# Performance work log

Measured on AMD Instinct MI355X. Metric: run time of the kernel, lower is better.

## Reference

```python
import jax, jax.numpy as jnp
import numpy as np

C = 256      # channels
H = 8        # num_heads
D = C // H   # head_dim = 32
B = 8        # packed segments (events)
LQ = 256     # queries per event
LKV = 1024   # kv tokens per event
EPS = float(np.finfo(np.float32).eps)  # torch RMSNorm default eps (None -> dtype eps)


def rmsnorm(x, w):
    # matches torch nn.RMSNorm (applied in fp32 in Block)
    return x * jax.lax.rsqrt(jnp.mean(x * x, axis=-1, keepdims=True) + EPS) * w


def setup_inputs() -> dict:
    key = jax.random.key(0)
    ks = jax.random.split(key, 20)
    Nq, Nkv = B * LQ, B * LKV
    def w(k, shape, scale=0.05):
        return jax.random.normal(k, shape, jnp.float32) * scale
    return {
        "q": jax.random.normal(ks[0], (Nq, C), jnp.float32),
        "kv": jax.random.normal(ks[1], (Nkv, C), jnp.float32),
        "pos_q": jax.random.normal(ks[2], (Nq, C), jnp.float32),
        "pos_k": jax.random.normal(ks[3], (Nkv, C), jnp.float32),
        # RMSNorm weights
        "w_norm_kv": jnp.ones((C,), jnp.float32),
        "w_norm1": jnp.ones((C,), jnp.float32),
        "w_norm2": jnp.ones((C,), jnp.float32),
        "w_norm3": jnp.ones((C,), jnp.float32),
        # cross-attention (q_proj/k_proj/v_proj no bias; out proj has bias)  W:[out,in]
        "ca_wq": w(ks[4], (C, C)), "ca_wk": w(ks[5], (C, C)), "ca_wv": w(ks[6], (C, C)),
        "ca_wo": w(ks[7], (C, C)), "ca_bo": jnp.zeros((C,), jnp.float32),
        # self-attention (q: [C,C]; kv fused: [2C,C]; out proj has bias)
        "sa_wq": w(ks[8], (C, C)), "sa_wkv": w(ks[9], (2 * C, C)),
        "sa_wo": w(ks[10], (C, C)), "sa_bo": jnp.zeros((C,), jnp.float32),
        # MLP (hidden = 4*C)
        "mlp_w1": w(ks[11], (4 * C, C)), "mlp_b1": jnp.zeros((4 * C,), jnp.float32),
        "mlp_w2": w(ks[12], (C, 4 * C)), "mlp_b2": jnp.zeros((C,), jnp.float32),
        # packed varlen metadata
        "cu_seqlens_q": jnp.arange(B + 1, dtype=jnp.int32) * LQ,
        "cu_seqlens_kv": jnp.arange(B + 1, dtype=jnp.int32) * LKV,
        "max_seqlen_q": LQ,
        "max_seqlen_kv": LKV,
    }


def reference(q, kv, pos_q, pos_k,
              w_norm_kv, w_norm1, w_norm2, w_norm3,
              ca_wq, ca_wk, ca_wv, ca_wo, ca_bo,
              sa_wq, sa_wkv, sa_wo, sa_bo,
              mlp_w1, mlp_b1, mlp_w2, mlp_b2,
              cu_seqlens_q, cu_seqlens_kv, max_seqlen_q, max_seqlen_kv):
    scale = D ** -0.5
    kv_n = rmsnorm(kv, w_norm_kv)

    # ---- cross-attention (use_attn_mask=False -> no mask, full packed attention) ----
    q_n = rmsnorm(q, w_norm1)
    qc = ((q_n + pos_q) @ ca_wq.T).reshape(-1, H, D)   # [Nq,H,D]
    kc = ((kv_n + pos_k) @ ca_wk.T).reshape(-1, H, D)  # [Nkv,H,D]
    vc = (kv_n @ ca_wv.T).reshape(-1, H, D)
    s = jnp.einsum('nhd,mhd->hnm', qc, kc) * scale     # [H,Nq,Nkv]
    feat = jnp.einsum('hnm,mhd->nhd', jax.nn.softmax(s, axis=-1), vc).reshape(-1, C)
    x = q + (feat @ ca_wo.T + ca_bo)

    # ---- self-attention with block-diagonal mask from cu_seqlens_q ----
    x_n = rmsnorm(x, w_norm2)
    qs = ((x_n + pos_q) @ sa_wq.T).reshape(-1, H, D)
    kvs = (x_n @ sa_wkv.T).reshape(-1, 2, H, D)
    ks_, vs = kvs[:, 0], kvs[:, 1]
    n = x.shape[0]
    seg = jnp.searchsorted(cu_seqlens_q[1:], jnp.arange(n, dtype=cu_seqlens_q.dtype), side='right')
    bias = jnp.where(seg[:, None] == seg[None, :], 0.0, -10000.0)  # [Nq,Nq]
    s2 = jnp.einsum('nhd,mhd->hnm', qs, ks_) * scale + bias
    feat2 = jnp.einsum('hnm,mhd->nhd', jax.nn.softmax(s2, axis=-1), vs).reshape(-1, C)
    x = x + (feat2 @ sa_wo.T + sa_bo)

    # ---- MLP (exact GELU, as torch nn.GELU default) ----
    x_n3 = rmsnorm(x, w_norm3)
    h = jax.nn.gelu(x_n3 @ mlp_w1.T + mlp_b1, approximate=False)
    x = x + (h @ mlp_w2.T + mlp_b2)
    return x
```

## Files before the change

### kernel.cpp

```cpp
#include <hip/hip_runtime.h>
#include <cmath>


#define EPS_F 1.1920928955078125e-07f

typedef __attribute__((ext_vector_type(8))) short short8;
typedef __attribute__((ext_vector_type(4))) short short4v;
typedef __attribute__((ext_vector_type(4))) float f32x4;

__device__ __forceinline__ unsigned short f2bf(float v) {
    union { float f; unsigned int u; } c; c.f = v;
    unsigned int r = c.u + 0x7FFFu + ((c.u >> 16) & 1u);
    return (unsigned short)(r >> 16);
}
__device__ __forceinline__ float bf2f(unsigned short u) {
    union { unsigned int u; float f; } c; c.u = ((unsigned int)u) << 16;
    return c.f;
}

struct WPtrs { const float* p[16]; };

__global__ __launch_bounds__(256) void cast_weights_kernel(
    WPtrs wp, unsigned short* __restrict__ outw)
{
    const int unit = blockIdx.x >> 5;
    const int off = ((blockIdx.x & 31) * 256 + threadIdx.x) * 8;
    const float* src = wp.p[unit];
    const float4 v0 = *(const float4*)(src + off);
    const float4 v1 = *(const float4*)(src + off + 4);
    short8 o;
    o[0] = (short)f2bf(v0.x); o[1] = (short)f2bf(v0.y);
    o[2] = (short)f2bf(v0.z); o[3] = (short)f2bf(v0.w);
    o[4] = (short)f2bf(v1.x); o[5] = (short)f2bf(v1.y);
    o[6] = (short)f2bf(v1.z); o[7] = (short)f2bf(v1.w);
    *(short8*)(outw + unit * 65536 + off) = o;
}

__global__ __launch_bounds__(256) void rmsnorm_dual_kernel(
    const float* __restrict__ X, const float* __restrict__ W,
    const float* __restrict__ pos, unsigned short* __restrict__ out_plain,
    unsigned short* __restrict__ out_pos)
{
    const int row = blockIdx.x;
    const int tid = threadIdx.x;
    const size_t base = (size_t)row * 256;
    const float v = X[base + tid];
    float sq = v * v;
    #pragma unroll
    for (int m = 1; m < 64; m <<= 1) sq += __shfl_xor(sq, m);
    __shared__ float ws4[4];
    if ((tid & 63) == 0) ws4[tid >> 6] = sq;
    __syncthreads();
    const float total = ws4[0] + ws4[1] + ws4[2] + ws4[3];
    const float ms = total * (1.0f / 256.0f) + EPS_F;
    float inv = rsqrtf(ms);
    inv = inv * (1.5f - 0.5f * ms * inv * inv);
    const float xn = v * inv * W[tid];
    if (out_plain) out_plain[base + tid] = f2bf(xn);
    if (out_pos)   out_pos[base + tid] = f2bf(xn + pos[base + tid]);
}

template<int ACT, int HAS_BIAS, int HAS_RES, int OUT_BF16>
__global__ __launch_bounds__(256) void gemm_bf16_kernel(
    const unsigned short* __restrict__ A, const unsigned short* __restrict__ Bw,
    const float* __restrict__ bias, const float* __restrict__ res,
    void* __restrict__ Cout, int M, int N, int K, float oscale)
{
    __shared__ __align__(16) char As[64 * 128];
    __shared__ __align__(16) char Bs[64 * 128];
    const int bm = blockIdx.x * 64, bn = blockIdx.y * 64;
    const int tid = threadIdx.x;
    const int w = tid >> 6, l = tid & 63;
    const int ql = l & 15, b = l >> 4;
    const int wr = w >> 1, wc = w & 1;

    f32x4 acc[2][2];
    #pragma unroll
    for (int m = 0; m < 2; ++m)
        #pragma unroll
        for (int n = 0; n < 2; ++n) acc[m][n] = (f32x4){0.f, 0.f, 0.f, 0.f};

    const int srow = tid >> 3;
    const int scolb = (tid & 7) * 16;
    const unsigned short* Ap0 = A + (size_t)(bm + srow) * K + (tid & 7) * 8;
    const unsigned short* Ap1 = A + (size_t)(bm + srow + 32) * K + (tid & 7) * 8;
    const unsigned short* Bp0 = Bw + (size_t)(bn + srow) * K + (tid & 7) * 8;
    const unsigned short* Bp1 = Bw + (size_t)(bn + srow + 32) * K + (tid & 7) * 8;
    const int sw0 = (srow * 128 + scolb) ^ ((srow & 7) << 4);
    const int sw1 = ((srow + 32) * 128 + scolb) ^ ((srow & 7) << 4);

    short8 ra0 = *(const short8*)(Ap0);
    short8 ra1 = *(const short8*)(Ap1);
    short8 rb0 = *(const short8*)(Bp0);
    short8 rb1 = *(const short8*)(Bp1);

    for (int k0 = 0; k0 < K; k0 += 64) {
        __syncthreads();
        *(short8*)(As + sw0) = ra0;
        *(short8*)(As + sw1) = ra1;
        *(short8*)(Bs + sw0) = rb0;
        *(short8*)(Bs + sw1) = rb1;
        if (k0 + 64 < K) {
            ra0 = *(const short8*)(Ap0 + k0 + 64);
            ra1 = *(const short8*)(Ap1 + k0 + 64);
            rb0 = *(const short8*)(Bp0 + k0 + 64);
            rb1 = *(const short8*)(Bp1 + k0 + 64);
        }
        __syncthreads();
        #pragma unroll
        for (int ks = 0; ks < 2; ++ks) {
            short8 af[2], bfr[2];
            #pragma unroll
            for (int m = 0; m < 2; ++m) {
                const int row = wr * 32 + m * 16 + ql;
                af[m] = *(const short8*)(As + ((row * 128 + ks * 64 + b * 16) ^ ((row & 7) << 4)));
            }
            #pragma unroll
            for (int n = 0; n < 2; ++n) {
                const int row = wc * 32 + n * 16 + ql;
                bfr[n] = *(const short8*)(Bs + ((row * 128 + ks * 64 + b * 16) ^ ((row & 7) << 4)));
            }
            #pragma unroll
            for (int m = 0; m < 2; ++m)
                #pragma unroll
                for (int n = 0; n < 2; ++n)
                    acc[m][n] = __builtin_amdgcn_mfma_f32_16x16x32_bf16(af[m], bfr[n], acc[m][n], 0, 0, 0);
        }
    }

    #pragma unroll
    for (int m = 0; m < 2; ++m) {
        #pragma unroll
        for (int n = 0; n < 2; ++n) {
            const int col = bn + wc * 32 + n * 16 + ql;
            #pragma unroll
            for (int r = 0; r < 4; ++r) {
                const int row = bm + wr * 32 + m * 16 + 4 * b + r;
                float v = acc[m][n][r];
                if (HAS_BIAS) v += bias[col];
                if (HAS_RES)  v += res[(size_t)row * N + col];
                if (ACT == 1) v = 0.5f * v * (1.0f + erff(v * 0.7071067811865476f));
                if (OUT_BF16)
                    ((unsigned short*)Cout)[(size_t)row * N + col] = f2bf(v * oscale);
                else
                    ((float*)Cout)[(size_t)row * N + col] = v;
            }
        }
    }
}

template<int SELF>
__global__ __launch_bounds__(256) void flash_mfma_kernel(
    const unsigned short* __restrict__ Qb, const unsigned short* __restrict__ Kb,
    const unsigned short* __restrict__ Vb, float* __restrict__ part_o,
    float* __restrict__ part_ml, unsigned short* __restrict__ out_bf,
    int kv_stride, int kv_per_split)
{
    __shared__ __align__(16) unsigned short Ks[64 * 32];
    __shared__ __align__(16) unsigned short Vt[32 * 64];
    const int qtile = blockIdx.x, h = blockIdx.y, split = blockIdx.z;
    const int tid = threadIdx.x;
    const int w = tid >> 6, l = tid & 63;
    const int ql = l & 15, b = l >> 4;
    const int qrow = qtile * 64 + w * 16 + ql;

    short8 qfrag = *(const short8*)(Qb + (size_t)qrow * 256 + h * 32 + b * 8);

    f32x4 oacc0 = {0.f, 0.f, 0.f, 0.f};
    f32x4 oacc1 = {0.f, 0.f, 0.f, 0.f};
    float m_run = -3.0e38f, l_part = 0.f;

    const int kv_base = SELF ? ((qtile >> 2) << 8) : split * kv_per_split;
    const int ntiles = kv_per_split / 64;
    const int skv = tid >> 2;
    const int sd8 = (tid & 3) * 8;

    for (int t = 0; t < ntiles; ++t) {
        const int kvg = kv_base + t * 64;
        short8 kin = *(const short8*)(Kb + (size_t)(kvg + skv) * kv_stride + h * 32 + sd8);
        short8 vin = *(const short8*)(Vb + (size_t)(kvg + skv) * kv_stride + h * 32 + sd8);
        __syncthreads();
        *(short8*)(Ks + skv * 32 + sd8) = kin;
        #pragma unroll
        for (int j = 0; j < 8; ++j) {
            const int d = sd8 + j;
            const int hh = (d + (d >> 3)) & 7;
            Vt[d * 64 + (skv ^ (hh << 3))] = (unsigned short)vin[j];
        }
        __syncthreads();

        f32x4 s[4];
        #pragma unroll
        for (int j = 0; j < 4; ++j) {
            short8 kfrag = *(const short8*)(Ks + (j * 16 + ql) * 32 + b * 8);
            f32x4 z = {0.f, 0.f, 0.f, 0.f};
            s[j] = __builtin_amdgcn_mfma_f32_16x16x32_bf16(kfrag, qfrag, z, 0, 0, 0);
        }

        float tmax = s[0][0];
        #pragma unroll
        for (int j = 0; j < 4; ++j)
            #pragma unroll
            for (int i = 0; i < 4; ++i) tmax = fmaxf(tmax, s[j][i]);
        tmax = fmaxf(tmax, __shfl_xor(tmax, 16));
        tmax = fmaxf(tmax, __shfl_xor(tmax, 32));
        const float newm = fmaxf(m_run, tmax);
        const float r = __expf(m_run - newm);
        m_run = newm;

        float p[4][4];
        float psum = 0.f;
        #pragma unroll
        for (int j = 0; j < 4; ++j)
            #pragma unroll
            for (int i = 0; i < 4; ++i) {
                p[j][i] = __expf(s[j][i] - newm);
                psum += p[j][i];
            }
        l_part = l_part * r + psum;
        #pragma unroll
        for (int i = 0; i < 4; ++i) { oacc0[i] *= r; oacc1[i] *= r; }

        short8 pf0, pf1;
        #pragma unroll
        for (int e = 0; e < 8; ++e) {
            pf0[e] = (short)f2bf(p[(e >> 2)][e & 3]);
            pf1[e] = (short)f2bf(p[2 + (e >> 2)][e & 3]);
        }

        #pragma unroll
        for (int tt = 0; tt < 2; ++tt) {
            const int d = 16 * tt + ql;
            const int hh = (d + (d >> 3)) & 7;
            #pragma unroll
            for (int c = 0; c < 2; ++c) {
                short4v lo = *(const short4v*)(Vt + d * 64 + ((32 * c + 4 * b) ^ (hh << 3)));
                short4v hi = *(const short4v*)(Vt + d * 64 + ((32 * c + 16 + 4 * b) ^ (hh << 3)));
                short8 vfrag;
                #pragma unroll
                for (int e = 0; e < 4; ++e) { vfrag[e] = lo[e]; vfrag[e + 4] = hi[e]; }
                if (tt == 0)
                    oacc0 = __builtin_amdgcn_mfma_f32_16x16x32_bf16(vfrag, (c == 0) ? pf0 : pf1, oacc0, 0, 0, 0);
                else
                    oacc1 = __builtin_amdgcn_mfma_f32_16x16x32_bf16(vfrag, (c == 0) ? pf0 : pf1, oacc1, 0, 0, 0);
            }
        }
    }

    float lsum = l_part;
    lsum += __shfl_xor(lsum, 16);
    lsum += __shfl_xor(lsum, 32);

    if (SELF) {
        const float invl = 1.0f / lsum;
        unsigned short* op = out_bf + (size_t)qrow * 256 + h * 32;
        #pragma unroll
        for (int i = 0; i < 4; ++i) {
            op[4 * b + i]      = f2bf(oacc0[i] * invl);
            op[16 + 4 * b + i] = f2bf(oacc1[i] * invl);
        }
    } else {
        const size_t obase = ((size_t)split * 2048 + qrow) * 256 + h * 32;
        *(float4*)(part_o + obase + 4 * b)      = make_float4(oacc0[0], oacc0[1], oacc0[2], oacc0[3]);
        *(float4*)(part_o + obase + 16 + 4 * b) = make_float4(oacc1[0], oacc1[1], oacc1[2], oacc1[3]);
        if (b == 0) {
            float* mlp = part_ml + (((size_t)split * 2048 + qrow) * 8 + h) * 2;
            mlp[0] = m_run; mlp[1] = lsum;
        }
    }
}

__global__ __launch_bounds__(256) void merge_kernel(
    const float* __restrict__ part_o, const float* __restrict__ part_ml,
    unsigned short* __restrict__ feat)
{
    const int row = blockIdx.x, c = threadIdx.x;
    const int h = c >> 5;
    float m_s[4], l_s[4];
    float M = -3.0e38f;
    #pragma unroll
    for (int s = 0; s < 4; ++s) {
        const float* mlp = part_ml + (((size_t)s * 2048 + row) * 8 + h) * 2;
        m_s[s] = mlp[0]; l_s[s] = mlp[1];
        M = fmaxf(M, m_s[s]);
    }
    float num = 0.f, den = 0.f;
    #pragma unroll
    for (int s = 0; s < 4; ++s) {
        const float wgt = __expf(m_s[s] - M);
        den += wgt * l_s[s];
        num += wgt * part_o[((size_t)s * 2048 + row) * 256 + c];
    }
    feat[(size_t)row * 256 + c] = f2bf(num / den);
}

extern "C" void kernel_launch(void* const* d_in, const int* in_sizes, int n_in,
                              void* d_out, int out_size, void* d_ws, size_t ws_size,
                              hipStream_t stream)
{
    const float* q         = (const float*)d_in[0];
    const float* kv        = (const float*)d_in[1];
    const float* pos_q     = (const float*)d_in[2];
    const float* pos_k     = (const float*)d_in[3];
    const float* w_norm_kv = (const float*)d_in[4];
    const float* w_norm1   = (const float*)d_in[5];
    const float* w_norm2   = (const float*)d_in[6];
    const float* w_norm3   = (const float*)d_in[7];
    const float* ca_wq     = (const float*)d_in[8];
    const float* ca_wk     = (const float*)d_in[9];
    const float* ca_wv     = (const float*)d_in[10];
    const float* ca_wo     = (const float*)d_in[11];
    const float* ca_bo     = (const float*)d_in[12];
    const float* sa_wq     = (const float*)d_in[13];
    const float* sa_wkv    = (const float*)d_in[14];
    const float* sa_wo     = (const float*)d_in[15];
    const float* sa_bo     = (const float*)d_in[16];
    const float* mlp_w1    = (const float*)d_in[17];
    const float* mlp_b1    = (const float*)d_in[18];
    const float* mlp_w2    = (const float*)d_in[19];
    const float* mlp_b2    = (const float*)d_in[20];
    float* out = (float*)d_out;
    float* ws  = (float*)d_ws;

    unsigned short* wbf      = (unsigned short*)(ws);
    unsigned short* kvn_bf   = (unsigned short*)(ws +  524288);
    unsigned short* kvpk_bf  = (unsigned short*)(ws + 1572864);
    unsigned short* kc_bf    = (unsigned short*)(ws + 2621440);
    unsigned short* vc_bf    = (unsigned short*)(ws + 3670016);
    unsigned short* qpn_bf   = (unsigned short*)(ws + 4718592);
    unsigned short* qc_bf    = (unsigned short*)(ws + 4980736);
    float*          part_o   = ws + 5242880;
    float*          part_ml  = ws + 7340032;
    unsigned short* feat_bf  = (unsigned short*)(ws + 7471104);
    float*          x        = ws + 7733248;
    unsigned short* xn2_bf   = (unsigned short*)(ws + 8257536);
    unsigned short* xn2p_bf  = (unsigned short*)(ws + 8519680);
    unsigned short* qs_bf    = (unsigned short*)(ws + 8781824);
    unsigned short* kvs_bf   = (unsigned short*)(ws + 9043968);
    unsigned short* feat2_bf = (unsigned short*)(ws + 9568256);
    float*          x2       = ws + 9830400;
    unsigned short* xn3_bf   = (unsigned short*)(ws + 10354688);
    unsigned short* hbuf_bf  = (unsigned short*)(ws + 10616832);

    unsigned short* wq_bf     = wbf;
    unsigned short* wk_bf     = wbf + 65536;
    unsigned short* wv_bf     = wbf + 131072;
    unsigned short* wo_bf     = wbf + 196608;
    unsigned short* sa_wq_bf  = wbf + 262144;
    unsigned short* sa_wkv_bf = wbf + 327680;
    unsigned short* sa_wo_bf  = wbf + 458752;
    unsigned short* mlp_w1_bf = wbf + 524288;
    unsigned short* mlp_w2_bf = wbf + 786432;

    WPtrs wp;
    wp.p[0] = ca_wq;  wp.p[1] = ca_wk;  wp.p[2] = ca_wv;  wp.p[3] = ca_wo;
    wp.p[4] = sa_wq;  wp.p[5] = sa_wkv; wp.p[6] = sa_wkv + 65536;
    wp.p[7] = sa_wo;
    wp.p[8] = mlp_w1;           wp.p[9]  = mlp_w1 + 65536;
    wp.p[10] = mlp_w1 + 131072; wp.p[11] = mlp_w1 + 196608;
    wp.p[12] = mlp_w2;          wp.p[13] = mlp_w2 + 65536;
    wp.p[14] = mlp_w2 + 131072; wp.p[15] = mlp_w2 + 196608;

    const float qscale = 0.17677669529663687f;

    cast_weights_kernel<<<512, 256, 0, stream>>>(wp, wbf);
    rmsnorm_dual_kernel<<<8192, 256, 0, stream>>>(kv, w_norm_kv, pos_k, kvn_bf, kvpk_bf);
    rmsnorm_dual_kernel<<<2048, 256, 0, stream>>>(q, w_norm1, pos_q, nullptr, qpn_bf);
    gemm_bf16_kernel<0,0,0,1><<<dim3( 32, 4), 256, 0, stream>>>(qpn_bf,  wq_bf, nullptr, nullptr, qc_bf, 2048, 256, 256, qscale);
    gemm_bf16_kernel<0,0,0,1><<<dim3(128, 4), 256, 0, stream>>>(kvpk_bf, wk_bf, nullptr, nullptr, kc_bf, 8192, 256, 256, 1.0f);
    gemm_bf16_kernel<0,0,0,1><<<dim3(128, 4), 256, 0, stream>>>(kvn_bf,  wv_bf, nullptr, nullptr, vc_bf, 8192, 256, 256, 1.0f);
    flash_mfma_kernel<0><<<dim3(32, 8, 4), 256, 0, stream>>>(qc_bf, kc_bf, vc_bf, part_o, part_ml, nullptr, 256, 2048);
    merge_kernel<<<2048, 256, 0, stream>>>(part_o, part_ml, feat_bf);
    gemm_bf16_kernel<0,1,1,0><<<dim3(32, 4), 256, 0, stream>>>(feat_bf, wo_bf, ca_bo, q, x, 2048, 256, 256, 1.0f);
    rmsnorm_dual_kernel<<<2048, 256, 0, stream>>>(x, w_norm2, pos_q, xn2_bf, xn2p_bf);
    gemm_bf16_kernel<0,0,0,1><<<dim3(32, 4), 256, 0, stream>>>(xn2p_bf, sa_wq_bf,  nullptr, nullptr, qs_bf,  2048, 256, 256, qscale);
    gemm_bf16_kernel<0,0,0,1><<<dim3(32, 8), 256, 0, stream>>>(xn2_bf,  sa_wkv_bf, nullptr, nullptr, kvs_bf, 2048, 512, 256, 1.0f);
    flash_mfma_kernel<1><<<dim3(32, 8, 1), 256, 0, stream>>>(qs_bf, kvs_bf, kvs_bf + 256, nullptr, nullptr, feat2_bf, 512, 256);
    gemm_bf16_kernel<0,1,1,0><<<dim3(32, 4), 256, 0, stream>>>(feat2_bf, sa_wo_bf, sa_bo, x, x2, 2048, 256, 256, 1.0f);
    rmsnorm_dual_kernel<<<2048, 256, 0, stream>>>(x2, w_norm3, nullptr, xn3_bf, nullptr);
    gemm_bf16_kernel<1,1,0,1><<<dim3(32,16), 256, 0, stream>>>(xn3_bf,  mlp_w1_bf, mlp_b1, nullptr, hbuf_bf, 2048, 1024, 256, 1.0f);
    gemm_bf16_kernel<0,1,1,0><<<dim3(32, 4), 256, 0, stream>>>(hbuf_bf, mlp_w2_bf, mlp_b2, x2, out, 2048, 256, 1024, 1.0f);
}
```

Measured before the change: 234.3 us.

## Pre-swizzle K/V into MFMA fragment layout, prefetch tiles, lazy rescale softmax

The K and V projection GEMMs now write their outputs directly in a per-head, per-64-token tile layout that matches the swizzled LDS fragment layout. The flash kernel can then copy tiles with plain 16-byte loads instead of doing a scalar transposed V scatter, and it prefetches the next tile into registers. The online softmax moves to exp2 with log2e folded into the query scale, and it skips the rescale when the max grows by no more than 8. The cross-attention KV split goes from 4 to 8, which doubles the partial buffers and the merge work. The costs are more scattered GEMM epilogue stores and a larger workspace.

```diff
diff --git a/kernel.cpp b/kernel.cpp
--- a/kernel.cpp
+++ b/kernel.cpp
@@ -1,11 +1,11 @@
 #include <hip/hip_runtime.h>
+#include <hip/hip_bf16.h>
 #include <cmath>
 
 
 #define EPS_F 1.1920928955078125e-07f
 
 typedef __attribute__((ext_vector_type(8))) short short8;
-typedef __attribute__((ext_vector_type(4))) short short4v;
 typedef __attribute__((ext_vector_type(4))) float f32x4;
 
 __device__ __forceinline__ unsigned short f2bf(float v) {
@@ -13,9 +13,27 @@
     unsigned int r = c.u + 0x7FFFu + ((c.u >> 16) & 1u);
     return (unsigned short)(r >> 16);
 }
-__device__ __forceinline__ float bf2f(unsigned short u) {
-    union { unsigned int u; float f; } c; c.u = ((unsigned int)u) << 16;
-    return c.f;
+__device__ __forceinline__ unsigned short f2bf_n(float v) {
+    union { __hip_bfloat16 h; unsigned short u; } cv;
+    cv.h = __float2bfloat16(v);
+    return cv.u;
+}
+
+__device__ __forceinline__ size_t kfrag_idx(int kv, int col, int Gk) {
+    const int h = col >> 5, d = col & 31;
+    const int g = kv >> 6, row = kv & 63;
+    const int idx = (row * 32 + d) ^ ((row & 7) << 3);
+    return ((size_t)(h * Gk + g)) * 2048 + idx;
+}
+__device__ __forceinline__ size_t vfrag_idx(int kv, int col, int Gk) {
+    const int h = col >> 5, d = col & 31;
+    const int tt = d >> 4, qd = d & 15;
+    const int g = kv >> 6, r6 = kv & 63;
+    const int c = r6 >> 5, r5 = r6 & 31;
+    const int hi = r5 >> 4, lo4 = r5 & 15;
+    const int b = lo4 >> 2, e = (hi << 2) | (lo4 & 3);
+    const int idx = tt * 1024 + ((qd * 64 + c * 32 + b * 8 + e) ^ ((qd & 7) << 3));
+    return ((size_t)(h * Gk + g)) * 2048 + idx;
 }
 
 struct WPtrs { const float* p[16]; };
@@ -60,11 +78,12 @@
     if (out_pos)   out_pos[base + tid] = f2bf(xn + pos[base + tid]);
 }
 
-template<int ACT, int HAS_BIAS, int HAS_RES, int OUT_BF16>
+template<int ACT, int HAS_BIAS, int HAS_RES, int STORE>
 __global__ __launch_bounds__(256) void gemm_bf16_kernel(
     const unsigned short* __restrict__ A, const unsigned short* __restrict__ Bw,
     const float* __restrict__ bias, const float* __restrict__ res,
-    void* __restrict__ Cout, int M, int N, int K, float oscale)
+    void* __restrict__ Cout, void* __restrict__ Cout2,
+    int M, int N, int K, float oscale, int Gk)
 {
     __shared__ __align__(16) char As[64 * 128];
     __shared__ __align__(16) char Bs[64 * 128];
@@ -140,10 +159,20 @@
                 if (HAS_BIAS) v += bias[col];
                 if (HAS_RES)  v += res[(size_t)row * N + col];
                 if (ACT == 1) v = 0.5f * v * (1.0f + erff(v * 0.7071067811865476f));
-                if (OUT_BF16)
+                if (STORE == 0)
+                    ((float*)Cout)[(size_t)row * N + col] = v;
+                else if (STORE == 1)
                     ((unsigned short*)Cout)[(size_t)row * N + col] = f2bf(v * oscale);
-                else
-                    ((float*)Cout)[(size_t)row * N + col] = v;
+                else if (STORE == 2)
+                    ((unsigned short*)Cout)[kfrag_idx(row, col, Gk)] = f2bf(v * oscale);
+                else if (STORE == 3)
+                    ((unsigned short*)Cout)[vfrag_idx(row, col, Gk)] = f2bf(v * oscale);
+                else {
+                    if (col < 256)
+                        ((unsigned short*)Cout)[kfrag_idx(row, col, Gk)] = f2bf(v);
+                    else
+                        ((unsigned short*)Cout2)[vfrag_idx(row, col - 256, Gk)] = f2bf(v);
+                }
             }
         }
     }
@@ -151,13 +180,13 @@
 
 template<int SELF>
 __global__ __launch_bounds__(256) void flash_mfma_kernel(
-    const unsigned short* __restrict__ Qb, const unsigned short* __restrict__ Kb,
-    const unsigned short* __restrict__ Vb, float* __restrict__ part_o,
+    const unsigned short* __restrict__ Qb, const unsigned short* __restrict__ Kp,
+    const unsigned short* __restrict__ Vp, float* __restrict__ part_o,
     float* __restrict__ part_ml, unsigned short* __restrict__ out_bf,
-    int kv_stride, int kv_per_split)
-{
-    __shared__ __align__(16) unsigned short Ks[64 * 32];
-    __shared__ __align__(16) unsigned short Vt[32 * 64];
+    int Gk, int ntiles)
+{
+    __shared__ __align__(16) unsigned short Kt[2048];
+    __shared__ __align__(16) unsigned short Vt[2048];
     const int qtile = blockIdx.x, h = blockIdx.y, split = blockIdx.z;
     const int tid = threadIdx.x;
     const int w = tid >> 6, l = tid & 63;
@@ -166,35 +195,38 @@
 
     short8 qfrag = *(const short8*)(Qb + (size_t)qrow * 256 + h * 32 + b * 8);
 
+    const int g0 = SELF ? ((qtile >> 2) << 2) : split * ntiles;
+    const unsigned short* Ksrc = Kp + ((size_t)(h * Gk + g0)) * 2048 + tid * 8;
+    const unsigned short* Vsrc = Vp + ((size_t)(h * Gk + g0)) * 2048 + tid * 8;
+
+    const int xsw = (ql & 7) << 3;
+    const int kb  = (ql * 32 + b * 8) ^ xsw;
+    const int vb0 = (ql * 64 + b * 8) ^ xsw;
+    const int vb1 = (ql * 64 + 32 + b * 8) ^ xsw;
+
     f32x4 oacc0 = {0.f, 0.f, 0.f, 0.f};
     f32x4 oacc1 = {0.f, 0.f, 0.f, 0.f};
     float m_run = -3.0e38f, l_part = 0.f;
 
-    const int kv_base = SELF ? ((qtile >> 2) << 8) : split * kv_per_split;
-    const int ntiles = kv_per_split / 64;
-    const int skv = tid >> 2;
-    const int sd8 = (tid & 3) * 8;
+    short8 kpre = *(const short8*)Ksrc;
+    short8 vpre = *(const short8*)Vsrc;
 
     for (int t = 0; t < ntiles; ++t) {
-        const int kvg = kv_base + t * 64;
-        short8 kin = *(const short8*)(Kb + (size_t)(kvg + skv) * kv_stride + h * 32 + sd8);
-        short8 vin = *(const short8*)(Vb + (size_t)(kvg + skv) * kv_stride + h * 32 + sd8);
         __syncthreads();
-        *(short8*)(Ks + skv * 32 + sd8) = kin;
-        #pragma unroll
-        for (int j = 0; j < 8; ++j) {
-            const int d = sd8 + j;
-            const int hh = (d + (d >> 3)) & 7;
-            Vt[d * 64 + (skv ^ (hh << 3))] = (unsigned short)vin[j];
+        *(short8*)(Kt + tid * 8) = kpre;
+        *(short8*)(Vt + tid * 8) = vpre;
+        if (t + 1 < ntiles) {
+            kpre = *(const short8*)(Ksrc + (size_t)(t + 1) * 2048);
+            vpre = *(const short8*)(Vsrc + (size_t)(t + 1) * 2048);
         }
         __syncthreads();
 
         f32x4 s[4];
         #pragma unroll
         for (int j = 0; j < 4; ++j) {
-            short8 kfrag = *(const short8*)(Ks + (j * 16 + ql) * 32 + b * 8);
+            short8 kf = *(const short8*)(Kt + kb + j * 512);
             f32x4 z = {0.f, 0.f, 0.f, 0.f};
-            s[j] = __builtin_amdgcn_mfma_f32_16x16x32_bf16(kfrag, qfrag, z, 0, 0, 0);
+            s[j] = __builtin_amdgcn_mfma_f32_16x16x32_bf16(kf, qfrag, z, 0, 0, 0);
         }
 
         float tmax = s[0][0];
@@ -204,9 +236,15 @@
             for (int i = 0; i < 4; ++i) tmax = fmaxf(tmax, s[j][i]);
         tmax = fmaxf(tmax, __shfl_xor(tmax, 16));
         tmax = fmaxf(tmax, __shfl_xor(tmax, 32));
-        const float newm = fmaxf(m_run, tmax);
-        const float r = __expf(m_run - newm);
-        m_run = newm;
+
+        if (!__all(tmax <= m_run + 8.f)) {
+            const float newm = fmaxf(m_run, tmax);
+            const float r = exp2f(m_run - newm);
+            l_part *= r;
+            #pragma unroll
+            for (int i = 0; i < 4; ++i) { oacc0[i] *= r; oacc1[i] *= r; }
+            m_run = newm;
+        }
 
         float p[4][4];
         float psum = 0.f;
@@ -214,37 +252,26 @@
         for (int j = 0; j < 4; ++j)
             #pragma unroll
             for (int i = 0; i < 4; ++i) {
-                p[j][i] = __expf(s[j][i] - newm);
+                p[j][i] = exp2f(s[j][i] - m_run);
                 psum += p[j][i];
             }
-        l_part = l_part * r + psum;
-        #pragma unroll
-        for (int i = 0; i < 4; ++i) { oacc0[i] *= r; oacc1[i] *= r; }
+        l_part += psum;
 
         short8 pf0, pf1;
         #pragma unroll
         for (int e = 0; e < 8; ++e) {
-            pf0[e] = (short)f2bf(p[(e >> 2)][e & 3]);
-            pf1[e] = (short)f2bf(p[2 + (e >> 2)][e & 3]);
-        }
-
-        #pragma unroll
-        for (int tt = 0; tt < 2; ++tt) {
-            const int d = 16 * tt + ql;
-            const int hh = (d + (d >> 3)) & 7;
-            #pragma unroll
-            for (int c = 0; c < 2; ++c) {
-                short4v lo = *(const short4v*)(Vt + d * 64 + ((32 * c + 4 * b) ^ (hh << 3)));
-                short4v hi = *(const short4v*)(Vt + d * 64 + ((32 * c + 16 + 4 * b) ^ (hh << 3)));
-                short8 vfrag;
-                #pragma unroll
-                for (int e = 0; e < 4; ++e) { vfrag[e] = lo[e]; vfrag[e + 4] = hi[e]; }
-                if (tt == 0)
-                    oacc0 = __builtin_amdgcn_mfma_f32_16x16x32_bf16(vfrag, (c == 0) ? pf0 : pf1, oacc0, 0, 0, 0);
-                else
-                    oacc1 = __builtin_amdgcn_mfma_f32_16x16x32_bf16(vfrag, (c == 0) ? pf0 : pf1, oacc1, 0, 0, 0);
-            }
-        }
+            pf0[e] = (short)f2bf_n(p[(e >> 2)][e & 3]);
+            pf1[e] = (short)f2bf_n(p[2 + (e >> 2)][e & 3]);
+        }
+
+        short8 v00 = *(const short8*)(Vt + vb0);
+        short8 v01 = *(const short8*)(Vt + vb1);
+        short8 v10 = *(const short8*)(Vt + 1024 + vb0);
+        short8 v11 = *(const short8*)(Vt + 1024 + vb1);
+        oacc0 = __builtin_amdgcn_mfma_f32_16x16x32_bf16(v00, pf0, oacc0, 0, 0, 0);
+        oacc0 = __builtin_amdgcn_mfma_f32_16x16x32_bf16(v01, pf1, oacc0, 0, 0, 0);
+        oacc1 = __builtin_amdgcn_mfma_f32_16x16x32_bf16(v10, pf0, oacc1, 0, 0, 0);
+        oacc1 = __builtin_amdgcn_mfma_f32_16x16x32_bf16(v11, pf1, oacc1, 0, 0, 0);
     }
 
     float lsum = l_part;
@@ -276,18 +303,18 @@
 {
     const int row = blockIdx.x, c = threadIdx.x;
     const int h = c >> 5;
-    float m_s[4], l_s[4];
+    float m_s[8], l_s[8];
     float M = -3.0e38f;
     #pragma unroll
-    for (int s = 0; s < 4; ++s) {
+    for (int s = 0; s < 8; ++s) {
         const float* mlp = part_ml + (((size_t)s * 2048 + row) * 8 + h) * 2;
         m_s[s] = mlp[0]; l_s[s] = mlp[1];
         M = fmaxf(M, m_s[s]);
     }
     float num = 0.f, den = 0.f;
     #pragma unroll
-    for (int s = 0; s < 4; ++s) {
-        const float wgt = __expf(m_s[s] - M);
+    for (int s = 0; s < 8; ++s) {
+        const float wgt = exp2f(m_s[s] - M);
         den += wgt * l_s[s];
         num += wgt * part_o[((size_t)s * 2048 + row) * 256 + c];
     }
@@ -323,24 +350,25 @@
     float* ws  = (float*)d_ws;
 
     unsigned short* wbf      = (unsigned short*)(ws);
-    unsigned short* kvn_bf   = (unsigned short*)(ws +  524288);
-    unsigned short* kvpk_bf  = (unsigned short*)(ws + 1572864);
-    unsigned short* kc_bf    = (unsigned short*)(ws + 2621440);
-    unsigned short* vc_bf    = (unsigned short*)(ws + 3670016);
-    unsigned short* qpn_bf   = (unsigned short*)(ws + 4718592);
-    unsigned short* qc_bf    = (unsigned short*)(ws + 4980736);
-    float*          part_o   = ws + 5242880;
-    float*          part_ml  = ws + 7340032;
-    unsigned short* feat_bf  = (unsigned short*)(ws + 7471104);
-    float*          x        = ws + 7733248;
-    unsigned short* xn2_bf   = (unsigned short*)(ws + 8257536);
-    unsigned short* xn2p_bf  = (unsigned short*)(ws + 8519680);
-    unsigned short* qs_bf    = (unsigned short*)(ws + 8781824);
-    unsigned short* kvs_bf   = (unsigned short*)(ws + 9043968);
-    unsigned short* feat2_bf = (unsigned short*)(ws + 9568256);
-    float*          x2       = ws + 9830400;
-    unsigned short* xn3_bf   = (unsigned short*)(ws + 10354688);
-    unsigned short* hbuf_bf  = (unsigned short*)(ws + 10616832);
+    unsigned short* kvn_bf   = (unsigned short*)(ws +   524288);
+    unsigned short* kvpk_bf  = (unsigned short*)(ws +  1572864);
+    unsigned short* kc_p     = (unsigned short*)(ws +  2621440);
+    unsigned short* vc_p     = (unsigned short*)(ws +  3670016);
+    unsigned short* qpn_bf   = (unsigned short*)(ws +  4718592);
+    unsigned short* qc_bf    = (unsigned short*)(ws +  4980736);
+    float*          part_o   = ws +  5242880;
+    float*          part_ml  = ws +  9437184;
+    unsigned short* feat_bf  = (unsigned short*)(ws +  9699328);
+    float*          x        = ws +  9961472;
+    unsigned short* xn2_bf   = (unsigned short*)(ws + 10485760);
+    unsigned short* xn2p_bf  = (unsigned short*)(ws + 10747904);
+    unsigned short* qs_bf    = (unsigned short*)(ws + 11010048);
+    unsigned short* kp_s     = (unsigned short*)(ws + 11272192);
+    unsigned short* vp_s     = (unsigned short*)(ws + 11534336);
+    unsigned short* feat2_bf = (unsigned short*)(ws + 11796480);
+    float*          x2       = ws + 12058624;
+    unsigned short* xn3_bf   = (unsigned short*)(ws + 12582912);
+    unsigned short* hbuf_bf  = (unsigned short*)(ws + 12845056);
 
     unsigned short* wq_bf     = wbf;
     unsigned short* wk_bf     = wbf + 65536;
@@ -361,23 +389,23 @@
     wp.p[12] = mlp_w2;          wp.p[13] = mlp_w2 + 65536;
     wp.p[14] = mlp_w2 + 131072; wp.p[15] = mlp_w2 + 196608;
 
-    const float qscale = 0.17677669529663687f;
+    const float qscale = 0.17677669529663687f * 1.4426950408889634f;
 
     cast_weights_kernel<<<512, 256, 0, stream>>>(wp, wbf);
     rmsnorm_dual_kernel<<<8192, 256, 0, stream>>>(kv, w_norm_kv, pos_k, kvn_bf, kvpk_bf);
     rmsnorm_dual_kernel<<<2048, 256, 0, stream>>>(q, w_norm1, pos_q, nullptr, qpn_bf);
-    gemm_bf16_kernel<0,0,0,1><<<dim3( 32, 4), 256, 0, stream>>>(qpn_bf,  wq_bf, nullptr, nullptr, qc_bf, 2048, 256, 256, qscale);
-    gemm_bf16_kernel<0,0,0,1><<<dim3(128, 4), 256, 0, stream>>>(kvpk_bf, wk_bf, nullptr, nullptr, kc_bf, 8192, 256, 256, 1.0f);
-    gemm_bf16_kernel<0,0,0,1><<<dim3(128, 4), 256, 0, stream>>>(kvn_bf,  wv_bf, nullptr, nullptr, vc_bf, 8192, 256, 256, 1.0f);
-    flash_mfma_kernel<0><<<dim3(32, 8, 4), 256, 0, stream>>>(qc_bf, kc_bf, vc_bf, part_o, part_ml, nullptr, 256, 2048);
+    gemm_bf16_kernel<0,0,0,1><<<dim3( 32, 4), 256, 0, stream>>>(qpn_bf,  wq_bf, nullptr, nullptr, qc_bf, nullptr, 2048, 256, 256, qscale, 0);
+    gemm_bf16_kernel<0,0,0,2><<<dim3(128, 4), 256, 0, stream>>>(kvpk_bf, wk_bf, nullptr, nullptr, kc_p,  nullptr, 8192, 256, 256, 1.0f, 128);
+    gemm_bf16_kernel<0,0,0,3><<<dim3(128, 4), 256, 0, stream>>>(kvn_bf,  wv_bf, nullptr, nullptr, vc_p,  nullptr, 8192, 256, 256, 1.0f, 128);
+    flash_mfma_kernel<0><<<dim3(32, 8, 8), 256, 0, stream>>>(qc_bf, kc_p, vc_p, part_o, part_ml, nullptr, 128, 16);
     merge_kernel<<<2048, 256, 0, stream>>>(part_o, part_ml, feat_bf);
-    gemm_bf16_kernel<0,1,1,0><<<dim3(32, 4), 256, 0, stream>>>(feat_bf, wo_bf, ca_bo, q, x, 2048, 256, 256, 1.0f);
+    gemm_bf16_kernel<0,1,1,0><<<dim3(32, 4), 256, 0, stream>>>(feat_bf, wo_bf, ca_bo, q, x, nullptr, 2048, 256, 256, 1.0f, 0);
     rmsnorm_dual_kernel<<<2048, 256, 0, stream>>>(x, w_norm2, pos_q, xn2_bf, xn2p_bf);
-    gemm_bf16_kernel<0,0,0,1><<<dim3(32, 4), 256, 0, stream>>>(xn2p_bf, sa_wq_bf,  nullptr, nullptr, qs_bf,  2048, 256, 256, qscale);
-    gemm_bf16_kernel<0,0,0,1><<<dim3(32, 8), 256, 0, stream>>>(xn2_bf,  sa_wkv_bf, nullptr, nullptr, kvs_bf, 2048, 512, 256, 1.0f);
-    flash_mfma_kernel<1><<<dim3(32, 8, 1), 256, 0, stream>>>(qs_bf, kvs_bf, kvs_bf + 256, nullptr, nullptr, feat2_bf, 512, 256);
-    gemm_bf16_kernel<0,1,1,0><<<dim3(32, 4), 256, 0, stream>>>(feat2_bf, sa_wo_bf, sa_bo, x, x2, 2048, 256, 256, 1.0f);
+    gemm_bf16_kernel<0,0,0,1><<<dim3(32, 4), 256, 0, stream>>>(xn2p_bf, sa_wq_bf,  nullptr, nullptr, qs_bf, nullptr, 2048, 256, 256, qscale, 0);
+    gemm_bf16_kernel<0,0,0,4><<<dim3(32, 8), 256, 0, stream>>>(xn2_bf,  sa_wkv_bf, nullptr, nullptr, kp_s,  vp_s,   2048, 512, 256, 1.0f, 32);
+    flash_mfma_kernel<1><<<dim3(32, 8, 1), 256, 0, stream>>>(qs_bf, kp_s, vp_s, nullptr, nullptr, feat2_bf, 32, 4);
+    gemm_bf16_kernel<0,1,1,0><<<dim3(32, 4), 256, 0, stream>>>(feat2_bf, sa_wo_bf, sa_bo, x, x2, nullptr, 2048, 256, 256, 1.0f, 0);
     rmsnorm_dual_kernel<<<2048, 256, 0, stream>>>(x2, w_norm3, nullptr, xn3_bf, nullptr);
-    gemm_bf16_kernel<1,1,0,1><<<dim3(32,16), 256, 0, stream>>>(xn3_bf,  mlp_w1_bf, mlp_b1, nullptr, hbuf_bf, 2048, 1024, 256, 1.0f);
-    gemm_bf16_kernel<0,1,1,0><<<dim3(32, 4), 256, 0, stream>>>(hbuf_bf, mlp_w2_bf, mlp_b2, x2, out, 2048, 256, 1024, 1.0f);
-}
+    gemm_bf16_kernel<1,1,0,1><<<dim3(32,16), 256, 0, stream>>>(xn3_bf,  mlp_w1_bf, mlp_b1, nullptr, hbuf_bf, nullptr, 2048, 1024, 256, 1.0f, 0);
+    gemm_bf16_kernel<0,1,1,0><<<dim3(32, 4), 256, 0, stream>>>(hbuf_bf, mlp_w2_bf, mlp_b2, x2, out, nullptr, 2048, 256, 1024, 1.0f, 0);
+}
```

After: 232.2 us. About the same (-0.9%).
